# Kernel optimization log

Hardware: AMD Instinct MI355X
Metric: run time of the kernel (lower is better)

## Reference

```python
import jax, jax.numpy as jnp
from jax import lax
import numpy as np

SEQ_LEN = 2048
BATCH = 512
HIDDEN = 256
CLASSES = 10


def setup_inputs() -> dict:
    key = jax.random.key(0)
    k1, k2, k3, k4 = jax.random.split(key, 4)
    return {
        "x": jax.random.normal(k1, (BATCH, SEQ_LEN), dtype=jnp.float32),
        "W_hx": jax.random.normal(k2, (HIDDEN, 1), dtype=jnp.float32),
        "W_hh": jax.random.normal(k3, (HIDDEN, HIDDEN), dtype=jnp.float32),
        "W_ph": jax.random.normal(k4, (CLASSES, HIDDEN), dtype=jnp.float32),
        "bias_h": jnp.zeros((HIDDEN, 1), dtype=jnp.float32),
        "bias_p": jnp.zeros((CLASSES,), dtype=jnp.float32),
    }


def reference(x, W_hx, W_hh, W_ph, bias_h, bias_p):
    # x: [B, T]. Hidden state h: [H, B]. Only last-step p is returned,
    # matching the torch loop where p is overwritten each iteration.
    B = x.shape[0]
    h0 = jnp.zeros((W_hh.shape[0], B), dtype=x.dtype)

    def step(h, x_t):  # x_t: [B]
        # W_hx @ x_t[None,:] : [H,1]@[1,B] -> [H,B]
        h_new = jnp.tanh(W_hx @ x_t[None, :] + W_hh @ h + bias_h)
        return h_new, None

    h_T, _ = lax.scan(step, h0, x.T)  # scan over time: x.T is [T, B]
    p = h_T.T @ W_ph.T + bias_p  # [B, C]
    return p
```

## Files before the change

kernel.cpp:

```cpp
#include <hip/hip_runtime.h>
#include <math.h>


#define TT 2048
#define BB 512
#define HH 256
#define CC 10
#define KH 128

__device__ __forceinline__ float ref_tanhf(float x)
{
    const float a1  = 4.89352455891786e-03f;
    const float a3  = 6.37261928875436e-04f;
    const float a5  = 1.48572235717979e-05f;
    const float a7  = 5.12229709037114e-08f;
    const float a9  = -8.60467152213735e-11f;
    const float a11 = 2.00018790482477e-13f;
    const float a13 = -2.76076847742355e-16f;
    const float b0  = 4.89352518554385e-03f;
    const float b2  = 2.26843463243900e-03f;
    const float b4  = 1.18534705686654e-04f;
    const float b6  = 1.19825839466702e-06f;

    const float kClamp = 7.99881172180175781f;
    const float xc = fmaxf(fminf(x, kClamp), -kClamp);
    const float x2 = __fmul_rn(xc, xc);
    float p = fmaf(x2, a13, a11);
    p = fmaf(x2, p, a9);
    p = fmaf(x2, p, a7);
    p = fmaf(x2, p, a5);
    p = fmaf(x2, p, a3);
    p = fmaf(x2, p, a1);
    p = __fmul_rn(xc, p);
    float q = fmaf(x2, b6, b4);
    q = fmaf(x2, q, b2);
    q = fmaf(x2, q, b0);
    const float r = __fdiv_rn(p, q);
    return (fabsf(x) < 0.0004f) ? x : r;
}

__global__ __launch_bounds__(512, 2)
void rnn_fwd(const float* __restrict__ x,
             const float* __restrict__ W_hx,
             const float* __restrict__ W_hh,
             const float* __restrict__ W_ph,
             const float* __restrict__ bias_h,
             const float* __restrict__ bias_p,
             float* __restrict__ out)
{
    const int tid   = threadIdx.x;
    const int group = tid >> 8;
    const int i     = tid & (HH - 1);
    const int b0    = blockIdx.x * 2;

    __shared__ __align__(16) float xls[2][TT];
    __shared__ __align__(16) float hbuf[2][2][HH];
    __shared__ __align__(16) float zpart[2][HH];

    float w[KH];
    const float* __restrict__ wrow = W_hh + (size_t)i * HH + group * KH;
#pragma unroll
    for (int k = 0; k < KH; k += 4) {
        const float4 v = *reinterpret_cast<const float4*>(wrow + k);
        w[k] = v.x; w[k + 1] = v.y; w[k + 2] = v.z; w[k + 3] = v.w;
    }
#pragma unroll
    for (int k = 0; k < KH; ++k) {
        asm volatile("" : "+v"(w[k]));
    }

    {
        const float4* __restrict__ xsrc =
            reinterpret_cast<const float4*>(x + (size_t)b0 * TT);
        float4* __restrict__ xdst = reinterpret_cast<float4*>(&xls[0][0]);
        xdst[tid]       = xsrc[tid];
        xdst[512 + tid] = xsrc[512 + tid];
    }
    const float whx = W_hx[i];
    const float bh  = bias_h[i];

    hbuf[group][1][i] = 0.0f;
    __syncthreads();

#define PBODY(COL, T, RP)                                                     \
    {                                                                         \
        const float* __restrict__ h = &hbuf[(COL)][(RP)][0];                  \
        float z = 0.0f;                                                       \
        _Pragma("unroll")                                                     \
        for (int k = 0; k < KH; k += 4) {                                     \
            const float4 h4 = *reinterpret_cast<const float4*>(h + k);        \
            z = fmaf(w[k],     h4.x, z);                                      \
            z = fmaf(w[k + 1], h4.y, z);                                      \
            z = fmaf(w[k + 2], h4.z, z);                                      \
            z = fmaf(w[k + 3], h4.w, z);                                      \
        }                                                                     \
        zpart[(COL)][i] = z;                                                  \
    }

#define QBODY(COL, T, RP)                                                     \
    {                                                                         \
        const float* __restrict__ h = &hbuf[(COL)][(RP)][0];                  \
        float z = zpart[(COL)][i];                                            \
        _Pragma("unroll")                                                     \
        for (int k = 0; k < KH; k += 4) {                                     \
            const float4 h4 = *reinterpret_cast<const float4*>(h + KH + k);   \
            z = fmaf(w[k],     h4.x, z);                                      \
            z = fmaf(w[k + 1], h4.y, z);                                      \
            z = fmaf(w[k + 2], h4.z, z);                                      \
            z = fmaf(w[k + 3], h4.w, z);                                      \
        }                                                                     \
        const float a0 = __fmul_rn(whx, xls[(COL)][(T)]);                     \
        z = __fadd_rn(__fadd_rn(a0, z), bh);                                  \
        hbuf[(COL)][(RP) ^ 1][i] = ref_tanhf(z);                              \
    }

#define STEP(U, RP)                                                           \
    {                                                                         \
        if (group == 0) { PBODY(0, (U), (RP)) }                               \
        else if ((U) >= 1) { QBODY(1, (U) - 1, (RP) ^ 1) }                    \
        __syncthreads();                                                      \
        if (group == 0) { PBODY(1, (U), (RP)) }                               \
        else { QBODY(0, (U), (RP)) }                                          \
        __syncthreads();                                                      \
    }

    STEP(0, 1)
    for (int u = 1; u + 1 < TT; u += 2) {
        STEP(u, 0)
        STEP(u + 1, 1)
    }
    STEP(TT - 1, 0)
    if (group == 1) { QBODY(1, TT - 1, 0) }
    __syncthreads();

#undef STEP
#undef QBODY
#undef PBODY

    if (tid < 2 * CC) {
        const int col = tid / CC;
        const int c   = tid % CC;
        const float* __restrict__ wp = W_ph + (size_t)c * HH;
        const float* __restrict__ hf = hbuf[col][1];
        float pv = 0.0f;
#pragma unroll 8
        for (int k = 0; k < HH; ++k) {
            pv = fmaf(hf[k], wp[k], pv);
        }
        out[(size_t)(b0 + col) * CC + c] = __fadd_rn(pv, bias_p[c]);
    }
}

extern "C" void kernel_launch(void* const* d_in, const int* in_sizes, int n_in,
                              void* d_out, int out_size, void* d_ws, size_t ws_size,
                              hipStream_t stream) {
    const float* x      = (const float*)d_in[0];
    const float* W_hx   = (const float*)d_in[1];
    const float* W_hh   = (const float*)d_in[2];
    const float* W_ph   = (const float*)d_in[3];
    const float* bias_h = (const float*)d_in[4];
    const float* bias_p = (const float*)d_in[5];
    float* out = (float*)d_out;

    rnn_fwd<<<dim3(BB / 2), dim3(512), 0, stream>>>(x, W_hx, W_hh, W_ph, bias_h, bias_p, out);
}
```

Baseline: 3.072 ms.

## Split K unevenly between groups and feed half of h via readlane broadcasts

The K range of the W_hh row is now split unevenly: the first group handles 136 columns and the second 120. Half of the hidden-state operands in each partial dot product are fetched with one per-lane LDS load, then broadcast through v_readlane instead of float4 LDS loads, which lowers LDS traffic per step. The time loop is rolled into a single loop with a runtime ping-pong index, and occupancy is now set through amdgpu_waves_per_eu. This trades LDS bandwidth for scalar readlane work and raises register pressure for the 136-entry weight array.

```diff
diff --git a/kernel.cpp b/kernel.cpp
--- a/kernel.cpp
+++ b/kernel.cpp
@@ -6,7 +6,8 @@
 #define BB 512
 #define HH 256
 #define CC 10
-#define KH 128
+#define KP 136
+#define KQ 120
 
 __device__ __forceinline__ float ref_tanhf(float x)
 {
@@ -39,7 +40,8 @@
     return (fabsf(x) < 0.0004f) ? x : r;
 }
 
-__global__ __launch_bounds__(512, 2)
+__global__ __launch_bounds__(512)
+__attribute__((amdgpu_waves_per_eu(2, 2)))
 void rnn_fwd(const float* __restrict__ x,
              const float* __restrict__ W_hx,
              const float* __restrict__ W_hh,
@@ -51,22 +53,38 @@
     const int tid   = threadIdx.x;
     const int group = tid >> 8;
     const int i     = tid & (HH - 1);
+    const int l     = tid & 63;
     const int b0    = blockIdx.x * 2;
 
     __shared__ __align__(16) float xls[2][TT];
     __shared__ __align__(16) float hbuf[2][2][HH];
     __shared__ __align__(16) float zpart[2][HH];
 
-    float w[KH];
-    const float* __restrict__ wrow = W_hh + (size_t)i * HH + group * KH;
+    float w[KP];
+    {
+        const float* __restrict__ wrow =
+            W_hh + (size_t)i * HH + (group ? KP : 0);
+        if (group == 0) {
 #pragma unroll
-    for (int k = 0; k < KH; k += 4) {
-        const float4 v = *reinterpret_cast<const float4*>(wrow + k);
-        w[k] = v.x; w[k + 1] = v.y; w[k + 2] = v.z; w[k + 3] = v.w;
-    }
+            for (int k = 0; k < KP; k += 4) {
+                const float4 v = *reinterpret_cast<const float4*>(wrow + k);
+                w[k] = v.x; w[k + 1] = v.y; w[k + 2] = v.z; w[k + 3] = v.w;
+            }
 #pragma unroll
-    for (int k = 0; k < KH; ++k) {
-        asm volatile("" : "+v"(w[k]));
+            for (int k = 0; k < KP; ++k) {
+                asm volatile("" : "+v"(w[k]));
+            }
+        } else {
+#pragma unroll
+            for (int k = 0; k < KQ; k += 4) {
+                const float4 v = *reinterpret_cast<const float4*>(wrow + k);
+                w[k] = v.x; w[k + 1] = v.y; w[k + 2] = v.z; w[k + 3] = v.w;
+            }
+#pragma unroll
+            for (int k = 0; k < KQ; ++k) {
+                asm volatile("" : "+v"(w[k]));
+            }
+        }
     }
 
     {
@@ -82,60 +100,74 @@
     hbuf[group][1][i] = 0.0f;
     __syncthreads();
 
-#define PBODY(COL, T, RP)                                                     \
+#define LDSB(J0, CNT, KS)                                                     \
+    _Pragma("unroll")                                                         \
+    for (int jj = 0; jj < (CNT); jj += 4) {                                   \
+        const float4 h4 =                                                     \
+            *reinterpret_cast<const float4*>(h + (KS) + (J0) + jj);           \
+        z = fmaf(w[(J0) + jj + 0], h4.x, z);                                  \
+        z = fmaf(w[(J0) + jj + 1], h4.y, z);                                  \
+        z = fmaf(w[(J0) + jj + 2], h4.z, z);                                  \
+        z = fmaf(w[(J0) + jj + 3], h4.w, z);                                  \
+    }
+
+#define RLB(J0, CNT, SRC, LOFF)                                               \
+    _Pragma("unroll")                                                         \
+    for (int jj = 0; jj < (CNT); ++jj) {                                      \
+        const float hv = __int_as_float(__builtin_amdgcn_readlane(            \
+            __float_as_int(SRC), (J0) + jj - (LOFF)));                        \
+        z = fmaf(w[(J0) + jj], hv, z);                                        \
+    }
+
+#define PBODY(COL, RP)                                                        \
     {                                                                         \
         const float* __restrict__ h = &hbuf[(COL)][(RP)][0];                  \
+        const float hA = h[l];                                                \
+        const float hB = h[64 + l];                                           \
         float z = 0.0f;                                                       \
-        _Pragma("unroll")                                                     \
-        for (int k = 0; k < KH; k += 4) {                                     \
-            const float4 h4 = *reinterpret_cast<const float4*>(h + k);        \
-            z = fmaf(w[k],     h4.x, z);                                      \
-            z = fmaf(w[k + 1], h4.y, z);                                      \
-            z = fmaf(w[k + 2], h4.z, z);                                      \
-            z = fmaf(w[k + 3], h4.w, z);                                      \
-        }                                                                     \
+        LDSB(0, 16, 0)   RLB(16, 16, hA, 0)                                   \
+        LDSB(32, 16, 0)  RLB(48, 16, hA, 0)                                   \
+        LDSB(64, 16, 0)  RLB(80, 16, hB, 64)                                  \
+        LDSB(96, 16, 0)  RLB(112, 16, hB, 64)                                 \
+        LDSB(128, 8, 0)                                                       \
         zpart[(COL)][i] = z;                                                  \
     }
 
 #define QBODY(COL, T, RP)                                                     \
     {                                                                         \
         const float* __restrict__ h = &hbuf[(COL)][(RP)][0];                  \
+        const float hD = h[136 + l];                                          \
+        const float hE = h[192 + l];                                          \
         float z = zpart[(COL)][i];                                            \
-        _Pragma("unroll")                                                     \
-        for (int k = 0; k < KH; k += 4) {                                     \
-            const float4 h4 = *reinterpret_cast<const float4*>(h + KH + k);   \
-            z = fmaf(w[k],     h4.x, z);                                      \
-            z = fmaf(w[k + 1], h4.y, z);                                      \
-            z = fmaf(w[k + 2], h4.z, z);                                      \
-            z = fmaf(w[k + 3], h4.w, z);                                      \
-        }                                                                     \
+        LDSB(0, 16, 136)  RLB(16, 16, hD, 0)                                  \
+        LDSB(32, 16, 136) RLB(48, 16, hD, 0)                                  \
+        LDSB(64, 16, 136) RLB(80, 16, hE, 56)                                 \
+        LDSB(96, 16, 136) RLB(112, 8, hE, 56)                                 \
         const float a0 = __fmul_rn(whx, xls[(COL)][(T)]);                     \
         z = __fadd_rn(__fadd_rn(a0, z), bh);                                  \
         hbuf[(COL)][(RP) ^ 1][i] = ref_tanhf(z);                              \
     }
 
-#define STEP(U, RP)                                                           \
-    {                                                                         \
-        if (group == 0) { PBODY(0, (U), (RP)) }                               \
-        else if ((U) >= 1) { QBODY(1, (U) - 1, (RP) ^ 1) }                    \
-        __syncthreads();                                                      \
-        if (group == 0) { PBODY(1, (U), (RP)) }                               \
-        else { QBODY(0, (U), (RP)) }                                          \
-        __syncthreads();                                                      \
+    if (group == 0) { PBODY(0, 1) }
+    __syncthreads();
+    if (group == 0) { PBODY(1, 1) } else { QBODY(0, 0, 1) }
+    __syncthreads();
+
+#pragma unroll 1
+    for (int u = 1; u < TT; ++u) {
+        const int rp = (u & 1) ^ 1;
+        if (group == 0) { PBODY(0, rp) } else { QBODY(1, u - 1, rp ^ 1) }
+        __syncthreads();
+        if (group == 0) { PBODY(1, rp) } else { QBODY(0, u, rp) }
+        __syncthreads();
     }
-
-    STEP(0, 1)
-    for (int u = 1; u + 1 < TT; u += 2) {
-        STEP(u, 0)
-        STEP(u + 1, 1)
-    }
-    STEP(TT - 1, 0)
     if (group == 1) { QBODY(1, TT - 1, 0) }
     __syncthreads();
 
-#undef STEP
 #undef QBODY
 #undef PBODY
+#undef RLB
+#undef LDSB
 
     if (tid < 2 * CC) {
         const int col = tid / CC;
```

Measured after the change: 3.838 ms. 1.25x slower.

## Broadcast hidden state via scalar loads from global workspace instead of LDS

Applied to the files above, without the earlier changes.

Moves the hidden-state double buffer from shared memory into a per-block global workspace and reads it with wave-uniform s_load_dwordx8 scalar loads, so the matvec uses SGPR operands instead of LDS float4 reads. The scalar cache is invalidated before each read so that values written by other threads are seen. The aim is to remove LDS read bandwidth and latency from the serial recurrence. The cost is that each step now round-trips through L2 with a cache invalidate, and correctness depends on vector stores reaching L2 before the barrier, which is not obviously guaranteed.

```diff
diff --git a/kernel.cpp b/kernel.cpp
--- a/kernel.cpp
+++ b/kernel.cpp
@@ -1,5 +1,6 @@
 #include <hip/hip_runtime.h>
 #include <math.h>
+#include <stdint.h>
 
 
 #define TT 2048
@@ -7,6 +8,8 @@
 #define HH 256
 #define CC 10
 #define KH 128
+
+typedef __attribute__((ext_vector_type(8))) int i8x;
 
 __device__ __forceinline__ float ref_tanhf(float x)
 {
@@ -46,7 +49,8 @@
              const float* __restrict__ W_ph,
              const float* __restrict__ bias_h,
              const float* __restrict__ bias_p,
-             float* __restrict__ out)
+             float* __restrict__ out,
+             float* __restrict__ ws)
 {
     const int tid   = threadIdx.x;
     const int group = tid >> 8;
@@ -54,8 +58,9 @@
     const int b0    = blockIdx.x * 2;
 
     __shared__ __align__(16) float xls[2][TT];
-    __shared__ __align__(16) float hbuf[2][2][HH];
     __shared__ __align__(16) float zpart[2][HH];
+
+    float* __restrict__ hg = ws + (size_t)blockIdx.x * (2 * 2 * HH);
 
     float w[KH];
     const float* __restrict__ wrow = W_hh + (size_t)i * HH + group * KH;
@@ -79,39 +84,76 @@
     const float whx = W_hx[i];
     const float bh  = bias_h[i];
 
-    hbuf[group][1][i] = 0.0f;
+    hg[(group * 2 + 1) * HH + i] = 0.0f;
     __syncthreads();
+
+#define KINV asm volatile("s_dcache_inv\n\ts_waitcnt lgkmcnt(0)" ::: "memory")
+
+#define SL(DST, IMM)                                                          \
+    asm volatile("s_load_dwordx8 %0, %1, " IMM                                \
+                 : "=s"(DST) : "s"(hb) : "memory")
+
+#define WAIT8(A, B, C, D, E, F, G, H)                                         \
+    asm volatile("s_waitcnt lgkmcnt(0)"                                       \
+                 : "+s"(A), "+s"(B), "+s"(C), "+s"(D),                        \
+                   "+s"(E), "+s"(F), "+s"(G), "+s"(H))
+
+#define FMA8(MT, K)                                                           \
+    z = fmaf(w[(K) + 0], __int_as_float(MT[0]), z);                           \
+    z = fmaf(w[(K) + 1], __int_as_float(MT[1]), z);                           \
+    z = fmaf(w[(K) + 2], __int_as_float(MT[2]), z);                           \
+    z = fmaf(w[(K) + 3], __int_as_float(MT[3]), z);                           \
+    z = fmaf(w[(K) + 4], __int_as_float(MT[4]), z);                           \
+    z = fmaf(w[(K) + 5], __int_as_float(MT[5]), z);                           \
+    z = fmaf(w[(K) + 6], __int_as_float(MT[6]), z);                           \
+    z = fmaf(w[(K) + 7], __int_as_float(MT[7]), z);
 
 #define PBODY(COL, T, RP)                                                     \
     {                                                                         \
-        const float* __restrict__ h = &hbuf[(COL)][(RP)][0];                  \
+        KINV;                                                                 \
+        const uint64_t hb =                                                   \
+            (uint64_t)(uintptr_t)(hg + ((COL) * 2 + (RP)) * HH);              \
+        i8x m0, m1, m2, m3, m4, m5, m6, m7;                                   \
+        i8x m8, m9, m10, m11, m12, m13, m14, m15;                             \
+        SL(m0, "0x00");  SL(m1, "0x20");  SL(m2, "0x40");  SL(m3, "0x60");    \
+        SL(m4, "0x80");  SL(m5, "0xA0");  SL(m6, "0xC0");  SL(m7, "0xE0");    \
         float z = 0.0f;                                                       \
-        _Pragma("unroll")                                                     \
-        for (int k = 0; k < KH; k += 4) {                                     \
-            const float4 h4 = *reinterpret_cast<const float4*>(h + k);        \
-            z = fmaf(w[k],     h4.x, z);                                      \
-            z = fmaf(w[k + 1], h4.y, z);                                      \
-            z = fmaf(w[k + 2], h4.z, z);                                      \
-            z = fmaf(w[k + 3], h4.w, z);                                      \
-        }                                                                     \
+        WAIT8(m0, m1, m2, m3, m4, m5, m6, m7);                                \
+        FMA8(m0, 0)   FMA8(m1, 8)   FMA8(m2, 16)  FMA8(m3, 24)                \
+        SL(m8, "0x100");  SL(m9, "0x120");                                    \
+        SL(m10, "0x140"); SL(m11, "0x160");                                   \
+        FMA8(m4, 32)  FMA8(m5, 40)  FMA8(m6, 48)  FMA8(m7, 56)                \
+        SL(m12, "0x180"); SL(m13, "0x1A0");                                   \
+        SL(m14, "0x1C0"); SL(m15, "0x1E0");                                   \
+        WAIT8(m8, m9, m10, m11, m12, m13, m14, m15);                          \
+        FMA8(m8, 64)  FMA8(m9, 72)  FMA8(m10, 80)  FMA8(m11, 88)              \
+        FMA8(m12, 96) FMA8(m13, 104) FMA8(m14, 112) FMA8(m15, 120)            \
         zpart[(COL)][i] = z;                                                  \
     }
 
 #define QBODY(COL, T, RP)                                                     \
     {                                                                         \
-        const float* __restrict__ h = &hbuf[(COL)][(RP)][0];                  \
+        KINV;                                                                 \
+        const uint64_t hb =                                                   \
+            (uint64_t)(uintptr_t)(hg + ((COL) * 2 + (RP)) * HH);              \
+        i8x m0, m1, m2, m3, m4, m5, m6, m7;                                   \
+        i8x m8, m9, m10, m11, m12, m13, m14, m15;                             \
+        SL(m0, "0x200"); SL(m1, "0x220"); SL(m2, "0x240"); SL(m3, "0x260");   \
+        SL(m4, "0x280"); SL(m5, "0x2A0"); SL(m6, "0x2C0"); SL(m7, "0x2E0");   \
         float z = zpart[(COL)][i];                                            \
-        _Pragma("unroll")                                                     \
-        for (int k = 0; k < KH; k += 4) {                                     \
-            const float4 h4 = *reinterpret_cast<const float4*>(h + KH + k);   \
-            z = fmaf(w[k],     h4.x, z);                                      \
-            z = fmaf(w[k + 1], h4.y, z);                                      \
-            z = fmaf(w[k + 2], h4.z, z);                                      \
-            z = fmaf(w[k + 3], h4.w, z);                                      \
-        }                                                                     \
+        WAIT8(m0, m1, m2, m3, m4, m5, m6, m7);                                \
+        FMA8(m0, 0)   FMA8(m1, 8)   FMA8(m2, 16)  FMA8(m3, 24)                \
+        SL(m8, "0x300");  SL(m9, "0x320");                                    \
+        SL(m10, "0x340"); SL(m11, "0x360");                                   \
+        FMA8(m4, 32)  FMA8(m5, 40)  FMA8(m6, 48)  FMA8(m7, 56)                \
+        SL(m12, "0x380"); SL(m13, "0x3A0");                                   \
+        SL(m14, "0x3C0"); SL(m15, "0x3E0");                                   \
+        WAIT8(m8, m9, m10, m11, m12, m13, m14, m15);                          \
+        FMA8(m8, 64)  FMA8(m9, 72)  FMA8(m10, 80)  FMA8(m11, 88)              \
+        FMA8(m12, 96) FMA8(m13, 104) FMA8(m14, 112) FMA8(m15, 120)            \
         const float a0 = __fmul_rn(whx, xls[(COL)][(T)]);                     \
         z = __fadd_rn(__fadd_rn(a0, z), bh);                                  \
-        hbuf[(COL)][(RP) ^ 1][i] = ref_tanhf(z);                              \
+        hg[((COL) * 2 + ((RP) ^ 1)) * HH + i] = ref_tanhf(z);                 \
     }
 
 #define STEP(U, RP)                                                           \
@@ -136,12 +178,16 @@
 #undef STEP
 #undef QBODY
 #undef PBODY
+#undef FMA8
+#undef WAIT8
+#undef SL
+#undef KINV
 
     if (tid < 2 * CC) {
         const int col = tid / CC;
         const int c   = tid % CC;
         const float* __restrict__ wp = W_ph + (size_t)c * HH;
-        const float* __restrict__ hf = hbuf[col][1];
+        const float* __restrict__ hf = hg + (col * 2 + 1) * HH;
         float pv = 0.0f;
 #pragma unroll 8
         for (int k = 0; k < HH; ++k) {
@@ -161,6 +207,8 @@
     const float* bias_h = (const float*)d_in[4];
     const float* bias_p = (const float*)d_in[5];
     float* out = (float*)d_out;
-
-    rnn_fwd<<<dim3(BB / 2), dim3(512), 0, stream>>>(x, W_hx, W_hh, W_ph, bias_h, bias_p, out);
+    float* ws  = (float*)d_ws;
+
+    rnn_fwd<<<dim3(BB / 2), dim3(512), 0, stream>>>(x, W_hx, W_hh, W_ph,
+                                                    bias_h, bias_p, out, ws);
 }
```

New measurement: 3.928 ms. 1.28x slower.
